# Performance work log

Hardware: AMD Instinct MI355X
Metric: run time of the kernel (lower is better)

Reference implementation:

```python
import jax, jax.numpy as jnp
import numpy as np

INPUT_LAYER_SIZE = 40960 * 2
LAYER1_SIZE = 512
LAYER2_SIZE = 32
LAYER3_SIZE = 32
BATCH = 4096


def setup_inputs() -> dict:
    key = jax.random.key(0)
    ks = jax.random.split(key, 10)
    # Sparse one-hot style features: mostly zeros with ~30 active entries per side.
    def sparse_features(k, n_active=30):
        kidx, = jax.random.split(k, 1)
        idx = jax.random.randint(kidx, (BATCH, n_active), 0, 40960)
        feats = jnp.zeros((BATCH, 40960), dtype=jnp.float32)
        return feats.at[jnp.arange(BATCH)[:, None], idx].set(1.0)
    w_features = sparse_features(ks[0])
    b_features = sparse_features(ks[1])
    s_in = 1.0 / np.sqrt(INPUT_LAYER_SIZE)
    s1 = 1.0 / np.sqrt(LAYER1_SIZE)
    s2 = 1.0 / np.sqrt(LAYER2_SIZE)
    s3 = 1.0 / np.sqrt(LAYER3_SIZE)
    return {
        "w_features": w_features,
        "b_features": b_features,
        "W_in": jax.random.uniform(ks[2], (LAYER1_SIZE, INPUT_LAYER_SIZE), jnp.float32, -s_in, s_in),
        "b_in": jax.random.uniform(ks[3], (LAYER1_SIZE,), jnp.float32, -s_in, s_in),
        "W1": jax.random.uniform(ks[4], (LAYER2_SIZE, LAYER1_SIZE), jnp.float32, -s1, s1),
        "b1": jax.random.uniform(ks[5], (LAYER2_SIZE,), jnp.float32, -s1, s1),
        "W2": jax.random.uniform(ks[6], (LAYER3_SIZE, LAYER2_SIZE), jnp.float32, -s2, s2),
        "b2": jax.random.uniform(ks[7], (LAYER3_SIZE,), jnp.float32, -s2, s2),
        "W3": jax.random.uniform(ks[8], (1, LAYER3_SIZE), jnp.float32, -s3, s3),
        "b3": jax.random.uniform(ks[9], (1,), jnp.float32, -s3, s3),
    }


def reference(w_features, b_features, W_in, b_in, W1, b1, W2, b2, W3, b3):
    # Concatenate both perspectives: [B, 81920]
    x = jnp.concatenate([w_features, b_features], axis=1)
    # Huge sparse-input accumulator layer (the kernel-headroom op)
    accum = x @ W_in.T + b_in                       # [B, 512]
    l1 = jnp.clip(accum, 0.0, 1.0)                  # clipped ReLU
    l2 = jnp.clip(l1 @ W1.T + b1, 0.0, 1.0)         # [B, 32]
    l3 = jnp.clip(l2 @ W2.T + b2, 0.0, 1.0)         # [B, 32]
    return l3 @ W3.T + b3                           # [B, 1]
```

## Files before the change

### kernel.cpp

```cpp
#include <hip/hip_runtime.h>
#include <hip/hip_bf16.h>

#define IN_PER_SIDE   40960
#define IN_TOTAL      81920
#define L1            512
#define L2            32
#define L3_           32
#define BATCH         4096

typedef float v4f __attribute__((ext_vector_type(4)));

__global__ __launch_bounds__(256) void transpose_win(
    const float* __restrict__ W, float* __restrict__ WT)
{
    __shared__ float tile[64][65];
    const int jt = blockIdx.x * 64;
    const int ot = blockIdx.y * 64;
    const int tx = threadIdx.x;
    const int ty = threadIdx.y;

#pragma unroll
    for (int k = 0; k < 4; ++k) {
        const int o = ty + 16 * k;
        const v4f* p = (const v4f*)&W[(size_t)(ot + o) * IN_TOTAL + jt + 4 * tx];
        v4f v = __builtin_nontemporal_load(p);
        tile[4 * tx + 0][o] = v.x;
        tile[4 * tx + 1][o] = v.y;
        tile[4 * tx + 2][o] = v.z;
        tile[4 * tx + 3][o] = v.w;
    }
    __syncthreads();
#pragma unroll
    for (int k = 0; k < 4; ++k) {
        const int j = ty + 16 * k;
        v4f v;
        v.x = tile[j][4 * tx + 0];
        v.y = tile[j][4 * tx + 1];
        v.z = tile[j][4 * tx + 2];
        v.w = tile[j][4 * tx + 3];
        *(v4f*)&WT[(size_t)(jt + j) * L1 + ot + 4 * tx] = v;
    }
}

__global__ __launch_bounds__(512) void nnue_fused(
    const float* __restrict__ wf, const float* __restrict__ bfeat,
    const float* __restrict__ WT, const float* __restrict__ W_in, int use_wt,
    const float* __restrict__ b_in,
    const float* __restrict__ W1, const float* __restrict__ b1,
    const float* __restrict__ W2, const float* __restrict__ b2,
    const float* __restrict__ W3, const float* __restrict__ b3,
    float* __restrict__ out)
{
    const int b = blockIdx.x;
    const int t = threadIdx.x;

    __shared__ int   idxs[128];
    __shared__ int   cnt;
    __shared__ float l1s[L1];
    __shared__ float l2acc[L2];
    __shared__ float l2s[L2];
    __shared__ float l3s[L3_];

    if (t == 0) cnt = 0;
    __syncthreads();

    const v4f* wrow = (const v4f*)(wf    + (size_t)b * IN_PER_SIDE);
    const v4f* brow = (const v4f*)(bfeat + (size_t)b * IN_PER_SIDE);
    const int nvec = IN_PER_SIDE / 4;

    for (int i = t; i < nvec; i += 512) {
        v4f v = __builtin_nontemporal_load(wrow + i);
        if (v.x != 0.0f) idxs[atomicAdd(&cnt, 1)] = 4 * i + 0;
        if (v.y != 0.0f) idxs[atomicAdd(&cnt, 1)] = 4 * i + 1;
        if (v.z != 0.0f) idxs[atomicAdd(&cnt, 1)] = 4 * i + 2;
        if (v.w != 0.0f) idxs[atomicAdd(&cnt, 1)] = 4 * i + 3;
        v4f u = __builtin_nontemporal_load(brow + i);
        if (u.x != 0.0f) idxs[atomicAdd(&cnt, 1)] = IN_PER_SIDE + 4 * i + 0;
        if (u.y != 0.0f) idxs[atomicAdd(&cnt, 1)] = IN_PER_SIDE + 4 * i + 1;
        if (u.z != 0.0f) idxs[atomicAdd(&cnt, 1)] = IN_PER_SIDE + 4 * i + 2;
        if (u.w != 0.0f) idxs[atomicAdd(&cnt, 1)] = IN_PER_SIDE + 4 * i + 3;
    }
    __syncthreads();

    const int n = cnt;
    float a0 = 0.0f, a1 = 0.0f, a2 = 0.0f, a3 = 0.0f;
    int i = 0;
    if (use_wt) {
        for (; i + 8 <= n; i += 8) {
            const float v0 = WT[(size_t)idxs[i + 0] * L1 + t];
            const float v1 = WT[(size_t)idxs[i + 1] * L1 + t];
            const float v2 = WT[(size_t)idxs[i + 2] * L1 + t];
            const float v3 = WT[(size_t)idxs[i + 3] * L1 + t];
            const float v4 = WT[(size_t)idxs[i + 4] * L1 + t];
            const float v5 = WT[(size_t)idxs[i + 5] * L1 + t];
            const float v6 = WT[(size_t)idxs[i + 6] * L1 + t];
            const float v7 = WT[(size_t)idxs[i + 7] * L1 + t];
            a0 += v0; a1 += v1; a2 += v2; a3 += v3;
            a0 += v4; a1 += v5; a2 += v6; a3 += v7;
        }
        for (; i < n; ++i) a0 += WT[(size_t)idxs[i] * L1 + t];
    } else {
        const float* wr = W_in + (size_t)t * IN_TOTAL;
        for (; i < n; ++i) a0 += wr[idxs[i]];
    }
    float acc = b_in[t] + ((a0 + a1) + (a2 + a3));
    l1s[t] = fminf(fmaxf(acc, 0.0f), 1.0f);
    __syncthreads();

    {
        const int k = t >> 4;
        const int g = t & 15;
        const float* w = W1 + (size_t)k * L1;
        float p = 0.0f;
        for (int o = g; o < L1; o += 16) p += w[o] * l1s[o];
#pragma unroll
        for (int off = 8; off > 0; off >>= 1) p += __shfl_down(p, off, 16);
        if (g == 0) l2acc[k] = p;
    }
    __syncthreads();
    if (t < L2) l2s[t] = fminf(fmaxf(l2acc[t] + b1[t], 0.0f), 1.0f);
    __syncthreads();

    if (t < L3_) {
        const float* w = W2 + (size_t)t * L2;
        float p = b2[t];
#pragma unroll
        for (int q = 0; q < L2; ++q) p += w[q] * l2s[q];
        l3s[t] = fminf(fmaxf(p, 0.0f), 1.0f);
    }
    __syncthreads();

    if (t == 0) {
        float p = b3[0];
#pragma unroll
        for (int q = 0; q < L3_; ++q) p += W3[q] * l3s[q];
        out[b] = p;
    }
}

extern "C" void kernel_launch(void* const* d_in, const int* in_sizes, int n_in,
                              void* d_out, int out_size, void* d_ws, size_t ws_size,
                              hipStream_t stream) {
    const float* wf   = (const float*)d_in[0];
    const float* bfeat= (const float*)d_in[1];
    const float* W_in = (const float*)d_in[2];
    const float* b_in = (const float*)d_in[3];
    const float* W1   = (const float*)d_in[4];
    const float* b1   = (const float*)d_in[5];
    const float* W2   = (const float*)d_in[6];
    const float* b2   = (const float*)d_in[7];
    const float* W3   = (const float*)d_in[8];
    const float* b3   = (const float*)d_in[9];
    float* out = (float*)d_out;

    const size_t wt_bytes = (size_t)IN_TOTAL * L1 * sizeof(float);
    const int use_wt = (ws_size >= wt_bytes) ? 1 : 0;
    float* WT = (float*)d_ws;

    if (use_wt) {
        dim3 grid(IN_TOTAL / 64, L1 / 64);
        dim3 block(16, 16);
        transpose_win<<<grid, block, 0, stream>>>(W_in, WT);
    }

    nnue_fused<<<BATCH, 512, 0, stream>>>(
        wf, bfeat, WT, W_in, use_wt, b_in, W1, b1, W2, b2, W3, b3, out);
}
```

Before: 1.412 ms.

## Merge weight transpose and feature index scan into one interleaved streaming kernel

Moves the dense feature scan out of the per-batch MLP kernel into a combined prep kernel whose blocks alternate between transposing W_in tiles and scanning one feature row per side. Sparse indices and counts go to workspace via global atomics, and a lean gather+MLP kernel then reads them. The goal is to overlap two bandwidth-bound streams, the weight transpose and the 1.3GB feature read, across the whole GPU, and to shrink the serial second kernel. In exchange it adds a memset launch, global atomics, and index round-trips through memory. A fallback path is kept for a small workspace.

```diff
diff --git a/kernel.cpp b/kernel.cpp
--- a/kernel.cpp
+++ b/kernel.cpp
@@ -7,44 +7,74 @@
 #define L2            32
 #define L3_           32
 #define BATCH         4096
+#define MAXIDX        128
 
 typedef float v4f __attribute__((ext_vector_type(4)));
 
-__global__ __launch_bounds__(256) void transpose_win(
-    const float* __restrict__ W, float* __restrict__ WT)
+#define WT_BYTES   ((size_t)IN_TOTAL * L1 * sizeof(float))
+#define CNT_BYTES  ((size_t)BATCH * sizeof(int))
+#define IDX_BYTES  ((size_t)BATCH * MAXIDX * sizeof(int))
+
+__global__ __launch_bounds__(256) void stream_prep(
+    const float* __restrict__ W, float* __restrict__ WT,
+    const float* __restrict__ wf, const float* __restrict__ bfeat,
+    int* __restrict__ cnt, int* __restrict__ idxs)
 {
     __shared__ float tile[64][65];
-    const int jt = blockIdx.x * 64;
-    const int ot = blockIdx.y * 64;
-    const int tx = threadIdx.x;
-    const int ty = threadIdx.y;
-
-#pragma unroll
-    for (int k = 0; k < 4; ++k) {
-        const int o = ty + 16 * k;
-        const v4f* p = (const v4f*)&W[(size_t)(ot + o) * IN_TOTAL + jt + 4 * tx];
-        v4f v = __builtin_nontemporal_load(p);
-        tile[4 * tx + 0][o] = v.x;
-        tile[4 * tx + 1][o] = v.y;
-        tile[4 * tx + 2][o] = v.z;
-        tile[4 * tx + 3][o] = v.w;
-    }
-    __syncthreads();
-#pragma unroll
-    for (int k = 0; k < 4; ++k) {
-        const int j = ty + 16 * k;
-        v4f v;
-        v.x = tile[j][4 * tx + 0];
-        v.y = tile[j][4 * tx + 1];
-        v.z = tile[j][4 * tx + 2];
-        v.w = tile[j][4 * tx + 3];
-        *(v4f*)&WT[(size_t)(jt + j) * L1 + ot + 4 * tx] = v;
-    }
-}
-
-__global__ __launch_bounds__(512) void nnue_fused(
-    const float* __restrict__ wf, const float* __restrict__ bfeat,
-    const float* __restrict__ WT, const float* __restrict__ W_in, int use_wt,
+    const int cls = blockIdx.x % 9;
+
+    if (cls < 5) {
+        const int tindex = (blockIdx.x / 9) * 5 + cls;
+        const int jt = (tindex % 1280) * 64;
+        const int ot = (tindex / 1280) * 64;
+        const int tx = threadIdx.x & 15;
+        const int ty = threadIdx.x >> 4;
+
+#pragma unroll
+        for (int k = 0; k < 4; ++k) {
+            const int o = ty + 16 * k;
+            const v4f* p = (const v4f*)&W[(size_t)(ot + o) * IN_TOTAL + jt + 4 * tx];
+            v4f v = __builtin_nontemporal_load(p);
+            tile[4 * tx + 0][o] = v.x;
+            tile[4 * tx + 1][o] = v.y;
+            tile[4 * tx + 2][o] = v.z;
+            tile[4 * tx + 3][o] = v.w;
+        }
+        __syncthreads();
+#pragma unroll
+        for (int k = 0; k < 4; ++k) {
+            const int j = ty + 16 * k;
+            v4f v;
+            v.x = tile[j][4 * tx + 0];
+            v.y = tile[j][4 * tx + 1];
+            v.z = tile[j][4 * tx + 2];
+            v.w = tile[j][4 * tx + 3];
+            *(v4f*)&WT[(size_t)(jt + j) * L1 + ot + 4 * tx] = v;
+        }
+    } else {
+        const int sindex = (blockIdx.x / 9) * 4 + (cls - 5);
+        const int row  = sindex >> 1;
+        const int side = sindex & 1;
+        const float* src = side ? bfeat : wf;
+        const int    bias = side ? IN_PER_SIDE : 0;
+        const v4f* p = (const v4f*)(src + (size_t)row * IN_PER_SIDE);
+        int* ic = cnt + row;
+        int* il = idxs + (size_t)row * MAXIDX;
+
+        const int nvec = IN_PER_SIDE / 4;
+        for (int i = threadIdx.x; i < nvec; i += 256) {
+            v4f v = __builtin_nontemporal_load(p + i);
+            if (v.x != 0.0f) il[atomicAdd(ic, 1)] = bias + 4 * i + 0;
+            if (v.y != 0.0f) il[atomicAdd(ic, 1)] = bias + 4 * i + 1;
+            if (v.z != 0.0f) il[atomicAdd(ic, 1)] = bias + 4 * i + 2;
+            if (v.w != 0.0f) il[atomicAdd(ic, 1)] = bias + 4 * i + 3;
+        }
+    }
+}
+
+__global__ __launch_bounds__(512) void gather_mlp(
+    const float* __restrict__ WT,
+    const int* __restrict__ cnt, const int* __restrict__ idxs,
     const float* __restrict__ b_in,
     const float* __restrict__ W1, const float* __restrict__ b1,
     const float* __restrict__ W2, const float* __restrict__ b2,
@@ -54,56 +84,34 @@
     const int b = blockIdx.x;
     const int t = threadIdx.x;
 
-    __shared__ int   idxs[128];
-    __shared__ int   cnt;
+    __shared__ int   sidx[MAXIDX];
     __shared__ float l1s[L1];
     __shared__ float l2acc[L2];
     __shared__ float l2s[L2];
     __shared__ float l3s[L3_];
 
-    if (t == 0) cnt = 0;
-    __syncthreads();
-
-    const v4f* wrow = (const v4f*)(wf    + (size_t)b * IN_PER_SIDE);
-    const v4f* brow = (const v4f*)(bfeat + (size_t)b * IN_PER_SIDE);
-    const int nvec = IN_PER_SIDE / 4;
-
-    for (int i = t; i < nvec; i += 512) {
-        v4f v = __builtin_nontemporal_load(wrow + i);
-        if (v.x != 0.0f) idxs[atomicAdd(&cnt, 1)] = 4 * i + 0;
-        if (v.y != 0.0f) idxs[atomicAdd(&cnt, 1)] = 4 * i + 1;
-        if (v.z != 0.0f) idxs[atomicAdd(&cnt, 1)] = 4 * i + 2;
-        if (v.w != 0.0f) idxs[atomicAdd(&cnt, 1)] = 4 * i + 3;
-        v4f u = __builtin_nontemporal_load(brow + i);
-        if (u.x != 0.0f) idxs[atomicAdd(&cnt, 1)] = IN_PER_SIDE + 4 * i + 0;
-        if (u.y != 0.0f) idxs[atomicAdd(&cnt, 1)] = IN_PER_SIDE + 4 * i + 1;
-        if (u.z != 0.0f) idxs[atomicAdd(&cnt, 1)] = IN_PER_SIDE + 4 * i + 2;
-        if (u.w != 0.0f) idxs[atomicAdd(&cnt, 1)] = IN_PER_SIDE + 4 * i + 3;
-    }
-    __syncthreads();
-
-    const int n = cnt;
+    const int n = cnt[b];
+    if (t < n) sidx[t] = idxs[(size_t)b * MAXIDX + t];
+    const float bias_t = b_in[t];
+    __syncthreads();
+
     float a0 = 0.0f, a1 = 0.0f, a2 = 0.0f, a3 = 0.0f;
     int i = 0;
-    if (use_wt) {
-        for (; i + 8 <= n; i += 8) {
-            const float v0 = WT[(size_t)idxs[i + 0] * L1 + t];
-            const float v1 = WT[(size_t)idxs[i + 1] * L1 + t];
-            const float v2 = WT[(size_t)idxs[i + 2] * L1 + t];
-            const float v3 = WT[(size_t)idxs[i + 3] * L1 + t];
-            const float v4 = WT[(size_t)idxs[i + 4] * L1 + t];
-            const float v5 = WT[(size_t)idxs[i + 5] * L1 + t];
-            const float v6 = WT[(size_t)idxs[i + 6] * L1 + t];
-            const float v7 = WT[(size_t)idxs[i + 7] * L1 + t];
-            a0 += v0; a1 += v1; a2 += v2; a3 += v3;
-            a0 += v4; a1 += v5; a2 += v6; a3 += v7;
-        }
-        for (; i < n; ++i) a0 += WT[(size_t)idxs[i] * L1 + t];
-    } else {
-        const float* wr = W_in + (size_t)t * IN_TOTAL;
-        for (; i < n; ++i) a0 += wr[idxs[i]];
-    }
-    float acc = b_in[t] + ((a0 + a1) + (a2 + a3));
+    for (; i + 8 <= n; i += 8) {
+        const float v0 = WT[(size_t)sidx[i + 0] * L1 + t];
+        const float v1 = WT[(size_t)sidx[i + 1] * L1 + t];
+        const float v2 = WT[(size_t)sidx[i + 2] * L1 + t];
+        const float v3 = WT[(size_t)sidx[i + 3] * L1 + t];
+        const float v4 = WT[(size_t)sidx[i + 4] * L1 + t];
+        const float v5 = WT[(size_t)sidx[i + 5] * L1 + t];
+        const float v6 = WT[(size_t)sidx[i + 6] * L1 + t];
+        const float v7 = WT[(size_t)sidx[i + 7] * L1 + t];
+        a0 += v0; a1 += v1; a2 += v2; a3 += v3;
+        a0 += v4; a1 += v5; a2 += v6; a3 += v7;
+    }
+    for (; i < n; ++i) a0 += WT[(size_t)sidx[i] * L1 + t];
+
+    float acc = bias_t + ((a0 + a1) + (a2 + a3));
     l1s[t] = fminf(fmaxf(acc, 0.0f), 1.0f);
     __syncthreads();
 
@@ -130,6 +138,75 @@
     }
     __syncthreads();
 
+    if (t == 0) {
+        float p = b3[0];
+#pragma unroll
+        for (int q = 0; q < L3_; ++q) p += W3[q] * l3s[q];
+        out[b] = p;
+    }
+}
+
+__global__ __launch_bounds__(512) void nnue_fallback(
+    const float* __restrict__ wf, const float* __restrict__ bfeat,
+    const float* __restrict__ W_in, const float* __restrict__ b_in,
+    const float* __restrict__ W1, const float* __restrict__ b1,
+    const float* __restrict__ W2, const float* __restrict__ b2,
+    const float* __restrict__ W3, const float* __restrict__ b3,
+    float* __restrict__ out)
+{
+    const int b = blockIdx.x;
+    const int t = threadIdx.x;
+    __shared__ int   idxs[MAXIDX];
+    __shared__ int   scnt;
+    __shared__ float l1s[L1];
+    __shared__ float l2acc[L2];
+    __shared__ float l2s[L2];
+    __shared__ float l3s[L3_];
+
+    if (t == 0) scnt = 0;
+    __syncthreads();
+    const v4f* wrow = (const v4f*)(wf    + (size_t)b * IN_PER_SIDE);
+    const v4f* brow = (const v4f*)(bfeat + (size_t)b * IN_PER_SIDE);
+    for (int i = t; i < IN_PER_SIDE / 4; i += 512) {
+        v4f v = wrow[i];
+        if (v.x != 0.0f) idxs[atomicAdd(&scnt, 1)] = 4 * i + 0;
+        if (v.y != 0.0f) idxs[atomicAdd(&scnt, 1)] = 4 * i + 1;
+        if (v.z != 0.0f) idxs[atomicAdd(&scnt, 1)] = 4 * i + 2;
+        if (v.w != 0.0f) idxs[atomicAdd(&scnt, 1)] = 4 * i + 3;
+        v4f u = brow[i];
+        if (u.x != 0.0f) idxs[atomicAdd(&scnt, 1)] = IN_PER_SIDE + 4 * i + 0;
+        if (u.y != 0.0f) idxs[atomicAdd(&scnt, 1)] = IN_PER_SIDE + 4 * i + 1;
+        if (u.z != 0.0f) idxs[atomicAdd(&scnt, 1)] = IN_PER_SIDE + 4 * i + 2;
+        if (u.w != 0.0f) idxs[atomicAdd(&scnt, 1)] = IN_PER_SIDE + 4 * i + 3;
+    }
+    __syncthreads();
+    const int n = scnt;
+    float a0 = 0.0f;
+    const float* wr = W_in + (size_t)t;
+    const float* row = W_in + (size_t)t * IN_TOTAL;
+    for (int i = 0; i < n; ++i) a0 += row[idxs[i]];
+    l1s[t] = fminf(fmaxf(b_in[t] + a0, 0.0f), 1.0f);
+    __syncthreads();
+    {
+        const int k = t >> 4, g = t & 15;
+        const float* w = W1 + (size_t)k * L1;
+        float p = 0.0f;
+        for (int o = g; o < L1; o += 16) p += w[o] * l1s[o];
+#pragma unroll
+        for (int off = 8; off > 0; off >>= 1) p += __shfl_down(p, off, 16);
+        if (g == 0) l2acc[k] = p;
+    }
+    __syncthreads();
+    if (t < L2) l2s[t] = fminf(fmaxf(l2acc[t] + b1[t], 0.0f), 1.0f);
+    __syncthreads();
+    if (t < L3_) {
+        const float* w = W2 + (size_t)t * L2;
+        float p = b2[t];
+#pragma unroll
+        for (int q = 0; q < L2; ++q) p += w[q] * l2s[q];
+        l3s[t] = fminf(fmaxf(p, 0.0f), 1.0f);
+    }
+    __syncthreads();
     if (t == 0) {
         float p = b3[0];
 #pragma unroll
@@ -153,16 +230,19 @@
     const float* b3   = (const float*)d_in[9];
     float* out = (float*)d_out;
 
-    const size_t wt_bytes = (size_t)IN_TOTAL * L1 * sizeof(float);
-    const int use_wt = (ws_size >= wt_bytes) ? 1 : 0;
-    float* WT = (float*)d_ws;
-
-    if (use_wt) {
-        dim3 grid(IN_TOTAL / 64, L1 / 64);
-        dim3 block(16, 16);
-        transpose_win<<<grid, block, 0, stream>>>(W_in, WT);
-    }
-
-    nnue_fused<<<BATCH, 512, 0, stream>>>(
-        wf, bfeat, WT, W_in, use_wt, b_in, W1, b1, W2, b2, W3, b3, out);
-}
+    const size_t need = WT_BYTES + CNT_BYTES + IDX_BYTES;
+    if (ws_size >= need) {
+        float* WT  = (float*)d_ws;
+        int*   cnt = (int*)((char*)d_ws + WT_BYTES);
+        int*   idx = (int*)((char*)d_ws + WT_BYTES + CNT_BYTES);
+
+        hipMemsetAsync(cnt, 0, CNT_BYTES, stream);
+
+        stream_prep<<<18432, 256, 0, stream>>>(W_in, WT, wf, bfeat, cnt, idx);
+        gather_mlp<<<BATCH, 512, 0, stream>>>(WT, cnt, idx, b_in,
+                                              W1, b1, W2, b2, W3, b3, out);
+    } else {
+        nnue_fallback<<<BATCH, 512, 0, stream>>>(
+            wf, bfeat, W_in, b_in, W1, b1, W2, b2, W3, b3, out);
+    }
+}
```

Result: slower. 1.454 ms (+3.0%).
